# Kernel tuning notes

Hardware: AMD Instinct MI355X
Metric: run time of the kernel (lower is better)

## Reference

```python
import jax, jax.numpy as jnp
import numpy as np

B, T, F, D = 128, 128, 128, 512
SCALE = 0.05  # keep relu-LSTM activations bounded with random weights


def setup_inputs() -> dict:
    key = jax.random.key(0)
    ks = jax.random.split(key, 16)
    n = jax.random.normal
    return {
        "enc_in": n(ks[0], (B, T, F), jnp.float32),
        "dec_in": n(ks[1], (B, T, F), jnp.float32),
        "enc_W0": n(ks[2], (F, 4 * D), jnp.float32) * SCALE,
        "enc_U0": n(ks[3], (D, 4 * D), jnp.float32) * SCALE,
        "enc_b0": jnp.zeros((4 * D,), jnp.float32),
        "enc_W1": n(ks[4], (D, 4 * D), jnp.float32) * SCALE,
        "enc_U1": n(ks[5], (D, 4 * D), jnp.float32) * SCALE,
        "enc_b1": jnp.zeros((4 * D,), jnp.float32),
        "dec_W0": n(ks[6], (F, 4 * D), jnp.float32) * SCALE,
        "dec_U0": n(ks[7], (D, 4 * D), jnp.float32) * SCALE,
        "dec_b0": jnp.zeros((4 * D,), jnp.float32),
        "dec_W1": n(ks[8], (D, 4 * D), jnp.float32) * SCALE,
        "dec_U1": n(ks[9], (D, 4 * D), jnp.float32) * SCALE,
        "dec_b1": jnp.zeros((4 * D,), jnp.float32),
        "dense_W": n(ks[10], (D, F), jnp.float32) * SCALE,
        "dense_b": jnp.zeros((F,), jnp.float32),
    }


def _lstm_cell(x, h, c, W, U, b):
    # Keras gate order: i, f, g(candidate), o; activation='relu', recurrent='sigmoid'
    z = x @ W + h @ U + b
    i, f, g, o = jnp.split(z, 4, axis=-1)
    i = jax.nn.sigmoid(i)
    f = jax.nn.sigmoid(f)
    g = jax.nn.relu(g)
    o = jax.nn.sigmoid(o)
    c2 = f * c + i * g
    h2 = o * jax.nn.relu(c2)
    return h2, c2


def reference(enc_in, dec_in, enc_W0, enc_U0, enc_b0, enc_W1, enc_U1, enc_b1,
              dec_W0, dec_U0, dec_b0, dec_W1, dec_U1, dec_b1, dense_W, dense_b):
    b, t, f = enc_in.shape
    d = enc_U0.shape[0]
    enc_params = [(enc_W0, enc_U0, enc_b0), (enc_W1, enc_U1, enc_b1)]
    dec_params = [(dec_W0, dec_U0, dec_b0), (dec_W1, dec_U1, dec_b1)]

    # Encoder: state (h, c) is shared/threaded across stacked layers, as in the source.
    def enc_step(carry, x_t):
        h, c = carry
        x = x_t
        for (W, U, bb) in enc_params:
            h, c = _lstm_cell(x, h, c, W, U, bb)
            x = h
        return (h, c), None

    h0 = jnp.zeros((b, d), enc_in.dtype)
    (h, c), _ = jax.lax.scan(enc_step, (h0, h0),
                             jnp.swapaxes(enc_in, 0, 1))  # [T,B,F]

    # every layer at a timestep gets the SAME initial state (previous timestep's
    # last-layer state), per the source code.
    def dec_step(carry, _):
        h, c, inp = carry
        cur = inp
        for (W, U, bb) in dec_params:
            h2, c2 = _lstm_cell(cur, h, c, W, U, bb)
            cur = h2
        out = cur @ dense_W + dense_b
        return (h2, c2, out), out

    inp0 = dec_in[:, 0, :]
    _, outs = jax.lax.scan(dec_step, (h, c, inp0), None, length=t)  # [T,B,F]
    outs = outs[::-1]  # source reverses all_outputs before concat
    return jnp.swapaxes(outs, 0, 1)  # [B,T,F]
```

## Files before the change

kernel.cpp:

```cpp
#include <hip/hip_runtime.h>


#define Bsz 128
#define Tsz 128
#define Fsz 128
#define Dsz 512
#define ND  2048
#define NBLK 256
#define NTHR 1024

#define OFF_HT0  1024
#define OFF_HT1  (OFF_HT0 + Dsz*Bsz)
#define OFF_HMT  (OFF_HT1 + Dsz*Bsz)
#define OFF_WEND (OFF_HMT + Dsz*Bsz)
#define OFF_P_EW0   OFF_WEND
#define OFF_P_EU0   (OFF_P_EW0 + Fsz*ND)
#define OFF_P_WSUM  (OFF_P_EU0 + Dsz*ND)
#define OFF_P_WDECA (OFF_P_WSUM + Dsz*ND)
#define OFF_P_DW0   (OFF_P_WDECA + Dsz*ND)
#define OFF_P_DU0   (OFF_P_DW0 + Fsz*ND)
#define OFF_P_DW1   (OFF_P_DU0 + Dsz*ND)
#define OFF_P_DU1   (OFF_P_DW1 + Dsz*ND)
#define OFF_P_BF    (OFF_P_DU1 + Dsz*ND)
#define OFF_P_DWT   (OFF_P_BF + ND)
#define WS_PACKED_FLOATS (OFF_P_DWT + Dsz*Fsz)
#define OFF_F_WSUM  OFF_WEND
#define OFF_F_WDECA (OFF_F_WSUM + Dsz*ND)
#define OFF_F_BF    (OFF_F_WDECA + Dsz*ND)
#define OFF_F_DWT   (OFF_F_BF + ND)
#define WS_FALLBACK_FLOATS (OFF_F_DWT + Dsz*Fsz)

#define NR 12

__device__ __forceinline__ float sigf(float x) {
    return 1.0f / (1.0f + __expf(-x));
}
__device__ __forceinline__ float ld_coh(const float* p) {
    return __hip_atomic_load((float*)p, __ATOMIC_RELAXED, __HIP_MEMORY_SCOPE_AGENT);
}
__device__ __forceinline__ void st_coh(float* p, float v) {
    __hip_atomic_store(p, v, __ATOMIC_RELAXED, __HIP_MEMORY_SCOPE_AGENT);
}

__device__ __forceinline__ void arrive(unsigned* slot, unsigned ep) {
    __syncthreads();
    if (threadIdx.x == 0)
        __hip_atomic_store(slot, ep, __ATOMIC_RELEASE, __HIP_MEMORY_SCOPE_AGENT);
}
__device__ __forceinline__ void wait_grp(unsigned* gslots, unsigned ep) {
    if (threadIdx.x < 64) {
        for (;;) {
            unsigned v = (threadIdx.x < 32)
                ? __hip_atomic_load(&gslots[threadIdx.x], __ATOMIC_RELAXED,
                                    __HIP_MEMORY_SCOPE_AGENT)
                : ep;
            if (__all(v >= ep)) break;
            __builtin_amdgcn_s_sleep(1);
        }
    }
    __syncthreads();
}
__device__ __forceinline__ void gbar_all(unsigned* slots, int blkid, unsigned ep) {
    __syncthreads();
    if (threadIdx.x == 0) {
        __threadfence();
        __hip_atomic_store(&slots[blkid], ep, __ATOMIC_RELEASE,
                           __HIP_MEMORY_SCOPE_AGENT);
    }
    if (threadIdx.x < 64) {
        for (;;) {
            unsigned mn = ~0u;
            #pragma unroll
            for (int q = 0; q < 4; ++q) {
                unsigned v = __hip_atomic_load(&slots[threadIdx.x * 4 + q],
                                               __ATOMIC_RELAXED, __HIP_MEMORY_SCOPE_AGENT);
                mn = min(mn, v);
            }
            if (__all(mn >= ep)) break;
            __builtin_amdgcn_s_sleep(1);
        }
        if (threadIdx.x == 0) __threadfence();
    }
    __syncthreads();
}

__device__ void pack_gate(float* dst, const float* src, int K, int kshift, int gid) {
    const int total = K * Dsz;
    for (int u = gid; u < total; u += NBLK * NTHR) {
        const int dd = u >> kshift;
        const int k = u & (K - 1);
        const float* sp = src + (size_t)k * ND + dd;
        ((float4*)dst)[u] = make_float4(sp[0], sp[Dsz], sp[2 * Dsz], sp[3 * Dsz]);
    }
}
__device__ void pack_wsum(float* dst, const float* a, const float* bsrc, int gid) {
    for (int u = gid; u < Dsz * Dsz; u += NBLK * NTHR) {
        const int dd = u >> 9, k = u & 511;
        const float* pa = a + (size_t)k * ND + dd;
        const float* pb = bsrc + (size_t)k * ND + dd;
        ((float4*)dst)[u] = make_float4(pa[0] + pb[0], pa[Dsz] + pb[Dsz],
                                        pa[2*Dsz] + pb[2*Dsz], pa[3*Dsz] + pb[3*Dsz]);
    }
}
__device__ void pack_wdeca_p(float* dst, const float* dU0, const float* dW0,
                             const float* dw, int gid) {
    for (int u = gid; u < Dsz * Dsz; u += NBLK * NTHR) {
        const int dd = u >> 9, k = u & 511;
        const float* pu = dU0 + (size_t)k * ND + dd;
        float a0 = pu[0], a1 = pu[Dsz], a2 = pu[2*Dsz], a3 = pu[3*Dsz];
        const float* dwr = dw + k * Fsz;
        for (int j = 0; j < Fsz; ++j) {
            const float wv = dwr[j];
            const float* dr = dW0 + (size_t)j * ND + dd;
            a0 += wv * dr[0]; a1 += wv * dr[Dsz];
            a2 += wv * dr[2*Dsz]; a3 += wv * dr[3*Dsz];
        }
        ((float4*)dst)[u] = make_float4(a0, a1, a2, a3);
    }
}


__device__ __forceinline__ void stageH9(float* XL, const float* HTsrc, int sr, int rbase) {
    #pragma unroll
    for (int ii = 0; ii < 4; ++ii) {
        const int i = (int)threadIdx.x + ii * NTHR;
        const int r = i >> 3, bb = i & 7;
        XL[(rbase + r) * NR + bb] = ld_coh(HTsrc + (size_t)r * Bsz + sr + bb);
    }
}
__device__ __forceinline__ void stageX9(float* XL, const float* src, int sr, int rbase) {
    const int r = (int)threadIdx.x & 127, bb = (int)threadIdx.x >> 7;
    XL[(rbase + r) * NR + bb] = src[(size_t)(sr + bb) * (Tsz * Fsz) + r];
}

#define FMA16(A0,A1,A2,A3,x4,w4) \
    A0.x += x4.x*w4.x; A0.y += x4.x*w4.y; A0.z += x4.x*w4.z; A0.w += x4.x*w4.w; \
    A1.x += x4.y*w4.x; A1.y += x4.y*w4.y; A1.z += x4.y*w4.z; A1.w += x4.y*w4.w; \
    A2.x += x4.z*w4.x; A2.y += x4.z*w4.y; A2.z += x4.z*w4.z; A2.w += x4.z*w4.w; \
    A3.x += x4.w*w4.x; A3.y += x4.w*w4.y; A3.z += x4.w*w4.z; A3.w += x4.w*w4.w;

template<int NJ>
__device__ __forceinline__ void consTv(const float4* __restrict__ Wp,
        const float* __restrict__ Xb,
        float4& A0, float4& A1, float4& A2, float4& A3)
{
    #pragma unroll 8
    for (int j = 0; j < NJ; ++j) {
        const float4 x4 = *(const float4*)(Xb + j * (32 * NR));
        const float4 w4 = Wp[j * 32];
        FMA16(A0, A1, A2, A3, x4, w4)
    }
}

__device__ __forceinline__ float dppx1(float v) {
    return v + __int_as_float(__builtin_amdgcn_mov_dpp(
        __float_as_int(v), 0xB1, 0xf, 0xf, true));
}
__device__ __forceinline__ float dppx2(float v) {
    return v + __int_as_float(__builtin_amdgcn_mov_dpp(
        __float_as_int(v), 0x4E, 0xf, 0xf, true));
}
__device__ __forceinline__ float dpphm(float v) {
    return v + __int_as_float(__builtin_amdgcn_mov_dpp(
        __float_as_int(v), 0x141, 0xf, 0xf, true));
}
#define HXCH(lo, hi, mask, cond) { \
    float s_ = (cond) ? (lo) : (hi); \
    float r_ = __shfl_xor(s_, mask); \
    if (cond) (hi) += r_; else (lo) += r_; }

__device__ __forceinline__ float4 redZ(float4 A0, float4 A1, float4 A2, float4 A3,
                                       bool khb, bool b3b)
{
    HXCH(A0.x, A2.x, 32, khb) HXCH(A0.y, A2.y, 32, khb)
    HXCH(A0.z, A2.z, 32, khb) HXCH(A0.w, A2.w, 32, khb)
    HXCH(A1.x, A3.x, 32, khb) HXCH(A1.y, A3.y, 32, khb)
    HXCH(A1.z, A3.z, 32, khb) HXCH(A1.w, A3.w, 32, khb)
    float4 B0, B1;
    B0.x = khb ? A2.x : A0.x; B0.y = khb ? A2.y : A0.y;
    B0.z = khb ? A2.z : A0.z; B0.w = khb ? A2.w : A0.w;
    B1.x = khb ? A3.x : A1.x; B1.y = khb ? A3.y : A1.y;
    B1.z = khb ? A3.z : A1.z; B1.w = khb ? A3.w : A1.w;
    HXCH(B0.x, B1.x, 8, b3b) HXCH(B0.y, B1.y, 8, b3b)
    HXCH(B0.z, B1.z, 8, b3b) HXCH(B0.w, B1.w, 8, b3b)
    float4 Z;
    Z.x = b3b ? B1.x : B0.x; Z.y = b3b ? B1.y : B0.y;
    Z.z = b3b ? B1.z : B0.z; Z.w = b3b ? B1.w : B0.w;
    Z.x = dppx1(Z.x); Z.y = dppx1(Z.y); Z.z = dppx1(Z.z); Z.w = dppx1(Z.w);
    Z.x = dppx2(Z.x); Z.y = dppx2(Z.y); Z.z = dppx2(Z.z); Z.w = dppx2(Z.w);
    Z.x = dpphm(Z.x); Z.y = dpphm(Z.y); Z.z = dpphm(Z.z); Z.w = dpphm(Z.w);
    return Z;
}

__device__ __forceinline__ float fin4b(float4 z, const float* bias, int dcol,
                                       float cprev, float& c2o) {
    float gi = sigf(z.x + bias[dcol]);
    float gf = sigf(z.y + bias[Dsz + dcol]);
    float gg = fmaxf(z.z + bias[2 * Dsz + dcol], 0.f);
    float go = sigf(z.w + bias[3 * Dsz + dcol]);
    float c2 = gf * cprev + gi * gg;
    c2o = c2;
    return go * fmaxf(c2, 0.f);
}

__device__ __forceinline__ void out_part9(const float* XL, const float* DWL, float* ORED,
                                          int xo, int koff, int wv,
                                          bool khb, bool b3b, bool own, int sown)
{
    const int ff = wv & 3, qk = wv >> 2;
    float o0 = 0.f, o1 = 0.f, o2 = 0.f, o3 = 0.f;
    const float* Xb = XL + qk * 128 * NR + xo;
    const float* Wb = DWL + ff * 512 + qk * 128 + koff;
    #pragma unroll
    for (int j = 0; j < 4; ++j) {
        const float4 x4 = *(const float4*)(Xb + j * (32 * NR));
        const float w = Wb[j * 32];
        o0 += x4.x * w; o1 += x4.y * w; o2 += x4.z * w; o3 += x4.w * w;
    }
    HXCH(o0, o2, 32, khb) HXCH(o1, o3, 32, khb)
    float p0 = khb ? o2 : o0;
    float p1 = khb ? o3 : o1;
    HXCH(p0, p1, 8, b3b)
    float o = b3b ? p1 : p0;
    o = dppx1(o); o = dppx2(o); o = dpphm(o);
    if (own) ORED[sown * 16 + ff * 4 + qk] = o;
}

__global__ void __launch_bounds__(NTHR, 1)
lstm_ae_v10(const float* enc_in, const float* dec_in,
            const float* eW0, const float* eU0, const float* eb0,
            const float* eW1, const float* eU1, const float* eb1,
            const float* dW0, const float* dU0, const float* db0,
            const float* dW1, const float* dU1, const float* db1,
            const float* dw, const float* db_, float* out, float* ws)
{
    __shared__ float XLA[1024 * NR];
    __shared__ float XLB[1024 * NR];
    __shared__ float DWL[4 * 512];
    __shared__ float OREDA[128];
    __shared__ float OREDB[128];

    unsigned* fslots = (unsigned*)ws;
    float* HT[2] = { ws + OFF_HT0, ws + OFF_HT1 };
    float* HMT = ws + OFF_HMT;

    const int blkid = blockIdx.x;
    const int grp  = blkid & 7;
    const int mem  = blkid >> 3;
    const int sgrp = mem & 7;
    const int dslc = mem >> 3;
    const int gm   = dslc * 8 + grp;
    const int chA  = sgrp * 2, chB = chA + 1;
    unsigned* gsA = (unsigned*)ws + 256 + chA * 32;
    unsigned* gsB = (unsigned*)ws + 256 + chB * 32;
    const int srA = sgrp * 16;
    const int srB = sgrp * 16 + 8;

    const int tid  = threadIdx.x;
    const int wv   = tid >> 6;
    const int lane = tid & 63;
    const int kh   = lane >> 5;
    const int qb2  = (lane >> 4) & 1;
    const int kc   = lane & 15;
    const int koff = kh * 16 + kc;
    const int dcol = grp * 64 + dslc * 16 + wv;
    const int fcol0 = grp * 16 + dslc * 4;
    const int gid  = blkid * NTHR + tid;
    const bool khb = (kh != 0);
    const bool b3b = ((kc & 8) != 0);
    const bool own = ((kc & 7) == 0);
    const int sown = qb2 * 4 + kh * 2 + ((kc >> 3) & 1);
    const int xo   = koff * NR + qb2 * 4;

    pack_gate(ws + OFF_P_EW0, eW0, Fsz, 7, gid);
    pack_gate(ws + OFF_P_EU0, eU0, Dsz, 9, gid);
    pack_wsum(ws + OFF_P_WSUM, eW1, eU1, gid);
    pack_wdeca_p(ws + OFF_P_WDECA, dU0, dW0, dw, gid);
    pack_gate(ws + OFF_P_DW0, dW0, Fsz, 7, gid);
    pack_gate(ws + OFF_P_DU0, dU0, Dsz, 9, gid);
    pack_gate(ws + OFF_P_DW1, dW1, Dsz, 9, gid);
    pack_gate(ws + OFF_P_DU1, dU1, Dsz, 9, gid);
    if (gid < ND) {
        float acc = db0[gid];
        for (int j = 0; j < Fsz; ++j) acc += db_[j] * dW0[(size_t)j * ND + gid];
        (ws + OFF_P_BF)[gid] = acc;
    }
    if (gid < Dsz * Fsz) {
        const int f = gid >> 9, k = gid & 511;
        (ws + OFF_P_DWT)[(size_t)f * Dsz + k] = dw[(size_t)k * Fsz + f];
    }
    gbar_all(fslots, blkid, 1);

    #pragma unroll
    for (int ii = 0; ii < 2; ++ii) {
        const int i = tid + ii * NTHR;
        DWL[i] = (ws + OFF_P_DWT)[(size_t)(fcol0 + (i >> 9)) * Dsz + (i & 511)];
    }
    __syncthreads();

    const float* pBF = ws + OFF_P_BF;
    const float4* W_EW0   = (const float4*)(ws + OFF_P_EW0)   + (size_t)dcol * 128 + koff;
    const float4* W_EU0   = (const float4*)(ws + OFF_P_EU0)   + (size_t)dcol * 512 + koff;
    const float4* W_WSUM  = (const float4*)(ws + OFF_P_WSUM)  + (size_t)dcol * 512 + koff;
    const float4* W_WDECA = (const float4*)(ws + OFF_P_WDECA) + (size_t)dcol * 512 + koff;
    const float4* W_DW0   = (const float4*)(ws + OFF_P_DW0)   + (size_t)dcol * 128 + koff;
    const float4* W_DU0   = (const float4*)(ws + OFF_P_DU0)   + (size_t)dcol * 512 + koff;
    const float4* W_DW1   = (const float4*)(ws + OFF_P_DW1)   + (size_t)dcol * 512 + koff;
    const float4* W_DU1   = (const float4*)(ws + OFF_P_DU1)   + (size_t)dcol * 512 + koff;

    unsigned epA = 0, epB = 0;
    int cur = 0;
    float cA = 0.f, cmA = 0.f, cB = 0.f, cmB = 0.f;
    const float4 Z4 = make_float4(0.f, 0.f, 0.f, 0.f);

    for (int t = 0; t < Tsz; ++t) {
        stageX9(XLA, enc_in + (size_t)t * Fsz, srA, 512);
        stageX9(XLB, enc_in + (size_t)t * Fsz, srB, 512);
        __syncthreads();
        {
            float4 A0 = Z4, A1 = Z4, A2 = Z4, A3 = Z4;
            consTv<4>(W_EW0, XLA + 512 * NR + xo, A0, A1, A2, A3);
            wait_grp(gsA, epA);
            stageH9(XLA, HT[cur], srA, 0);
            __syncthreads();
            consTv<16>(W_EU0, XLA + xo, A0, A1, A2, A3);
            float4 Z = redZ(A0, A1, A2, A3, khb, b3b);
            if (own) {
                float cn; float h2 = fin4b(Z, eb0, dcol, cA, cn); cmA = cn;
                st_coh(&HMT[(size_t)dcol * Bsz + srA + sown], h2);
            }
            arrive(&gsA[gm], ++epA);
        }
        {
            float4 A0 = Z4, A1 = Z4, A2 = Z4, A3 = Z4;
            consTv<4>(W_EW0, XLB + 512 * NR + xo, A0, A1, A2, A3);
            wait_grp(gsB, epB);
            stageH9(XLB, HT[cur], srB, 0);
            __syncthreads();
            consTv<16>(W_EU0, XLB + xo, A0, A1, A2, A3);
            float4 Z = redZ(A0, A1, A2, A3, khb, b3b);
            if (own) {
                float cn; float h2 = fin4b(Z, eb0, dcol, cB, cn); cmB = cn;
                st_coh(&HMT[(size_t)dcol * Bsz + srB + sown], h2);
            }
            arrive(&gsB[gm], ++epB);
        }
        {
            wait_grp(gsA, epA);
            stageH9(XLA, HMT, srA, 0);
            __syncthreads();
            float4 A0 = Z4, A1 = Z4, A2 = Z4, A3 = Z4;
            consTv<16>(W_WSUM, XLA + xo, A0, A1, A2, A3);
            float4 Z = redZ(A0, A1, A2, A3, khb, b3b);
            if (own) {
                float cn; float h2 = fin4b(Z, eb1, dcol, cmA, cn); cA = cn;
                st_coh(&HT[cur ^ 1][(size_t)dcol * Bsz + srA + sown], h2);
            }
            arrive(&gsA[gm], ++epA);
        }
        {
            wait_grp(gsB, epB);
            stageH9(XLB, HMT, srB, 0);
            __syncthreads();
            float4 A0 = Z4, A1 = Z4, A2 = Z4, A3 = Z4;
            consTv<16>(W_WSUM, XLB + xo, A0, A1, A2, A3);
            float4 Z = redZ(A0, A1, A2, A3, khb, b3b);
            if (own) {
                float cn; float h2 = fin4b(Z, eb1, dcol, cmB, cn); cB = cn;
                st_coh(&HT[cur ^ 1][(size_t)dcol * Bsz + srB + sown], h2);
            }
            arrive(&gsB[gm], ++epB);
        }
        cur ^= 1;
    }

    {
        stageX9(XLA, dec_in, srA, 512);
        stageX9(XLB, dec_in, srB, 512);
        __syncthreads();
        {
            float4 A0 = Z4, A1 = Z4, A2 = Z4, A3 = Z4;
            consTv<4>(W_DW0, XLA + 512 * NR + xo, A0, A1, A2, A3);
            wait_grp(gsA, epA);
            stageH9(XLA, HT[cur], srA, 0);
            __syncthreads();
            consTv<16>(W_DU0, XLA + xo, A0, A1, A2, A3);
            float4 Z = redZ(A0, A1, A2, A3, khb, b3b);
            if (own) {
                float cd; float h2 = fin4b(Z, db0, dcol, cA, cd);
                st_coh(&HMT[(size_t)dcol * Bsz + srA + sown], h2);
            }
            arrive(&gsA[gm], ++epA);
        }
        {
            float4 A0 = Z4, A1 = Z4, A2 = Z4, A3 = Z4;
            consTv<4>(W_DW0, XLB + 512 * NR + xo, A0, A1, A2, A3);
            wait_grp(gsB, epB);
            stageH9(XLB, HT[cur], srB, 0);
            __syncthreads();
            consTv<16>(W_DU0, XLB + xo, A0, A1, A2, A3);
            float4 Z = redZ(A0, A1, A2, A3, khb, b3b);
            if (own) {
                float cd; float h2 = fin4b(Z, db0, dcol, cB, cd);
                st_coh(&HMT[(size_t)dcol * Bsz + srB + sown], h2);
            }
            arrive(&gsB[gm], ++epB);
        }
        {
            wait_grp(gsA, epA);
            stageH9(XLA, HMT, srA, 512);
            __syncthreads();
            float4 A0 = Z4, A1 = Z4, A2 = Z4, A3 = Z4;
            consTv<16>(W_DU1, XLA + xo, A0, A1, A2, A3);
            consTv<16>(W_DW1, XLA + 512 * NR + xo, A0, A1, A2, A3);
            float4 Z = redZ(A0, A1, A2, A3, khb, b3b);
            if (own) {
                float cn; float h2 = fin4b(Z, db1, dcol, cA, cn); cA = cn;
                st_coh(&HT[cur ^ 1][(size_t)dcol * Bsz + srA + sown], h2);
            }
            arrive(&gsA[gm], ++epA);
        }
        {
            wait_grp(gsB, epB);
            stageH9(XLB, HMT, srB, 512);
            __syncthreads();
            float4 A0 = Z4, A1 = Z4, A2 = Z4, A3 = Z4;
            consTv<16>(W_DU1, XLB + xo, A0, A1, A2, A3);
            consTv<16>(W_DW1, XLB + 512 * NR + xo, A0, A1, A2, A3);
            float4 Z = redZ(A0, A1, A2, A3, khb, b3b);
            if (own) {
                float cn; float h2 = fin4b(Z, db1, dcol, cB, cn); cB = cn;
                st_coh(&HT[cur ^ 1][(size_t)dcol * Bsz + srB + sown], h2);
            }
            arrive(&gsB[gm], ++epB);
        }
        cur ^= 1;
    }

    for (int t = 1; t < Tsz; ++t) {
        const int tt = Tsz - t;
        {
            wait_grp(gsA, epA);
            stageH9(XLA, HT[cur], srA, 0);
            __syncthreads();
            float4 A0 = Z4, A1 = Z4, A2 = Z4, A3 = Z4;
            consTv<16>(W_WDECA, XLA + xo, A0, A1, A2, A3);
            out_part9(XLA, DWL, OREDA, xo, koff, wv, khb, b3b, own, sown);
            float4 Z = redZ(A0, A1, A2, A3, khb, b3b);
            if (own) {
                float cd; float h2 = fin4b(Z, pBF, dcol, cA, cd);
                st_coh(&HMT[(size_t)dcol * Bsz + srA + sown], h2);
            }
            arrive(&gsA[gm], ++epA);
            if (tid < 32) {
                const int bb = tid >> 2, ff = tid & 3;
                const int fc = fcol0 + ff;
                const float* r = OREDA + bb * 16 + ff * 4;
                float s = r[0] + r[1] + r[2] + r[3] + db_[fc];
                out[((size_t)(srA + bb) * Tsz + tt) * Fsz + fc] = s;
            }
        }
        {
            wait_grp(gsB, epB);
            stageH9(XLB, HT[cur], srB, 0);
            __syncthreads();
            float4 A0 = Z4, A1 = Z4, A2 = Z4, A3 = Z4;
            consTv<16>(W_WDECA, XLB + xo, A0, A1, A2, A3);
            out_part9(XLB, DWL, OREDB, xo, koff, wv, khb, b3b, own, sown);
            float4 Z = redZ(A0, A1, A2, A3, khb, b3b);
            if (own) {
                float cd; float h2 = fin4b(Z, pBF, dcol, cB, cd);
                st_coh(&HMT[(size_t)dcol * Bsz + srB + sown], h2);
            }
            arrive(&gsB[gm], ++epB);
            if (tid < 32) {
                const int bb = tid >> 2, ff = tid & 3;
                const int fc = fcol0 + ff;
                const float* r = OREDB + bb * 16 + ff * 4;
                float s = r[0] + r[1] + r[2] + r[3] + db_[fc];
                out[((size_t)(srB + bb) * Tsz + tt) * Fsz + fc] = s;
            }
        }
        {
            wait_grp(gsA, epA);
            stageH9(XLA, HMT, srA, 512);
            __syncthreads();
            float4 A0 = Z4, A1 = Z4, A2 = Z4, A3 = Z4;
            consTv<16>(W_DU1, XLA + xo, A0, A1, A2, A3);
            consTv<16>(W_DW1, XLA + 512 * NR + xo, A0, A1, A2, A3);
            float4 Z = redZ(A0, A1, A2, A3, khb, b3b);
            if (own) {
                float cn; float h2 = fin4b(Z, db1, dcol, cA, cn); cA = cn;
                st_coh(&HT[cur ^ 1][(size_t)dcol * Bsz + srA + sown], h2);
            }
            arrive(&gsA[gm], ++epA);
        }
        {
            wait_grp(gsB, epB);
            stageH9(XLB, HMT, srB, 512);
            __syncthreads();
            float4 A0 = Z4, A1 = Z4, A2 = Z4, A3 = Z4;
            consTv<16>(W_DU1, XLB + xo, A0, A1, A2, A3);
            consTv<16>(W_DW1, XLB + 512 * NR + xo, A0, A1, A2, A3);
            float4 Z = redZ(A0, A1, A2, A3, khb, b3b);
            if (own) {
                float cn; float h2 = fin4b(Z, db1, dcol, cB, cn); cB = cn;
                st_coh(&HT[cur ^ 1][(size_t)dcol * Bsz + srB + sown], h2);
            }
            arrive(&gsB[gm], ++epB);
        }
        cur ^= 1;
    }

    wait_grp(gsA, epA);
    stageH9(XLA, HT[cur], srA, 0);
    __syncthreads();
    out_part9(XLA, DWL, OREDA, xo, koff, wv, khb, b3b, own, sown);
    wait_grp(gsB, epB);
    stageH9(XLB, HT[cur], srB, 0);
    __syncthreads();
    out_part9(XLB, DWL, OREDB, xo, koff, wv, khb, b3b, own, sown);
    __syncthreads();
    if (tid < 64) {
        const int half = tid >> 5;
        const int l = tid & 31;
        const int bb = l >> 2, ff = l & 3;
        const int fc = fcol0 + ff;
        const float* ored = half ? OREDB : OREDA;
        const int sr = half ? srB : srA;
        const float* r = ored + bb * 16 + ff * 4;
        float s = r[0] + r[1] + r[2] + r[3] + db_[fc];
        out[((size_t)(sr + bb) * Tsz + 0) * Fsz + fc] = s;
    }
}


__device__ __forceinline__ void stage_vec(float* XL, int xstr, int dstoff,
        const float* src, int row0, int ld, int klen, int c4shift) {
    const int q = klen >> 2;
    const int n4 = q * 16;
    for (int i = threadIdx.x; i < n4; i += NTHR) {
        const int row = i >> c4shift;
        const int c4 = i & (q - 1);
        float4 v = *(const float4*)(src + (size_t)(row0 + row) * ld + (c4 << 2));
        *(float4*)(XL + row * xstr + dstoff + (c4 << 2)) = v;
    }
}
__device__ __forceinline__ void stage_coh_T(float* XL, int xstr, int dstoff,
        const float* HTsrc, int row0) {
    for (int i = threadIdx.x; i < Dsz * 16; i += NTHR) {
        const int d = i >> 4;
        const int bb = i & 15;
        XL[bb * xstr + dstoff + d] = ld_coh(HTsrc + (size_t)d * Bsz + row0 + bb);
    }
}
__device__ __forceinline__ void acc_segS(float4& z, const float* xp,
                                         const float* W, int kbase, int ksub, int dcol) {
    for (int j = 0; j < ksub; ++j) {
        const float x = xp[j];
        const float* wr = W + (size_t)(kbase + j) * ND + dcol;
        z.x += x * wr[0];
        z.y += x * wr[Dsz];
        z.z += x * wr[2 * Dsz];
        z.w += x * wr[3 * Dsz];
    }
}
__device__ __forceinline__ void reduce4(float4& z) {
    z.x += __shfl_xor(z.x, 16); z.x += __shfl_xor(z.x, 32);
    z.y += __shfl_xor(z.y, 16); z.y += __shfl_xor(z.y, 32);
    z.z += __shfl_xor(z.z, 16); z.z += __shfl_xor(z.z, 32);
    z.w += __shfl_xor(z.w, 16); z.w += __shfl_xor(z.w, 32);
}
__device__ __forceinline__ float lstm_fin(float4 z, const float* bias, int dcol,
                                          float cprev, float& c2out) {
    float gi = sigf(z.x + bias[dcol]);
    float gf = sigf(z.y + bias[Dsz + dcol]);
    float gg = fmaxf(z.z + bias[2 * Dsz + dcol], 0.f);
    float go = sigf(z.w + bias[3 * Dsz + dcol]);
    float c2 = gf * cprev + gi * gg;
    c2out = c2;
    return go * fmaxf(c2, 0.f);
}
__device__ __forceinline__ void out_part(const float* XL, int xstr, float* ORED,
                                         int b, int kc, int w, int fcol,
                                         const float* dwT) {
    const int q = w >> 2;
    const float* xp = XL + b * xstr + q * 128 + kc * 32;
    const float* wt = dwT + (size_t)fcol * Dsz + q * 128 + kc * 32;
    float acc = 0.f;
    #pragma unroll
    for (int j = 0; j < 32; j += 4) {
        float4 x4 = *(const float4*)(xp + j);
        float4 w4 = *(const float4*)(wt + j);
        acc += x4.x * w4.x + x4.y * w4.y + x4.z * w4.z + x4.w * w4.w;
    }
    acc += __shfl_xor(acc, 16); acc += __shfl_xor(acc, 32);
    if ((threadIdx.x & 63) < 16) ORED[b * 16 + (w & 3) * 4 + q] = acc;
}

__global__ void __launch_bounds__(NTHR, 1)
lstm_ae_fb(const float* enc_in, const float* dec_in,
           const float* eW0, const float* eU0, const float* eb0,
           const float* eW1, const float* eU1, const float* eb1,
           const float* dW0, const float* dU0, const float* db0,
           const float* dW1, const float* dU1, const float* db1,
           const float* dw, const float* db_, float* out, float* ws)
{
    __shared__ float XL[16 * 1028];
    __shared__ float ORED[256];

    unsigned* fslots = (unsigned*)ws;
    float* HT[2] = { ws + OFF_HT0, ws + OFF_HT1 };
    float* HMT = ws + OFF_HMT;

    const int blkid = blockIdx.x;
    const int grp  = blkid & 7;
    const int mem  = blkid >> 3;
    const int sgrp = mem & 7;
    const int dslc = mem >> 3;
    const int gm   = dslc * 8 + grp;
    unsigned* gslots = (unsigned*)ws + 256 + sgrp * 64;

    const int tid  = threadIdx.x;
    const int w    = tid >> 6;
    const int lane = tid & 63;
    const int b    = lane & 15;
    const int kc   = lane >> 4;
    const int dcol = grp * 64 + dslc * 16 + w;
    const int bgl  = sgrp * 16 + b;
    const int row0 = sgrp * 16;
    const int fcol = grp * 16 + dslc * 4 + (w & 3);
    const int gid  = blkid * NTHR + tid;

    pack_wsum(ws + OFF_F_WSUM, eW1, eU1, gid);
    pack_wdeca_p(ws + OFF_F_WDECA, dU0, dW0, dw, gid);
    if (gid < ND) {
        float acc = db0[gid];
        for (int j = 0; j < Fsz; ++j) acc += db_[j] * dW0[(size_t)j * ND + gid];
        (ws + OFF_F_BF)[gid] = acc;
    }
    if (gid < Dsz * Fsz) {
        const int f = gid >> 9, k = gid & 511;
        (ws + OFF_F_DWT)[(size_t)f * Dsz + k] = dw[(size_t)k * Fsz + f];
    }
    const float* pWSUM = ws + OFF_F_WSUM;
    const float* pWDECA = ws + OFF_F_WDECA;
    const float* pBF = ws + OFF_F_BF;
    const float* pDWT = ws + OFF_F_DWT;
    gbar_all(fslots, blkid, 1);

    unsigned ep = 0;
    int cur = 0;
    float c_car = 0.f;

    for (int t = 0; t < Tsz; ++t) {
        stage_vec(XL, 644, 0, enc_in + (size_t)t * Fsz, row0, Tsz * Fsz, 128, 5);
        __syncthreads();
        float4 z = make_float4(0.f, 0.f, 0.f, 0.f);
        acc_segS(z, XL + b * 644 + kc * 32, eW0, kc * 32, 32, dcol);
        wait_grp(gslots, ep);
        stage_coh_T(XL, 644, 128, HT[cur], row0);
        __syncthreads();
        acc_segS(z, XL + b * 644 + 128 + kc * 128, eU0, kc * 128, 128, dcol);
        reduce4(z);
        float c1 = 0.f;
        if (lane < 16) {
            float h2 = lstm_fin(z, eb0, dcol, c_car, c1);
            st_coh(&HMT[(size_t)dcol * Bsz + bgl], h2);
        }
        arrive(&gslots[gm], ++ep);
        wait_grp(gslots, ep);
        stage_coh_T(XL, 516, 0, HMT, row0);
        __syncthreads();
        z = make_float4(0.f, 0.f, 0.f, 0.f);
        {
            const float4* wp = (const float4*)pWSUM + (size_t)dcol * 512 + kc * 128;
            const float* xp = XL + b * 516 + kc * 128;
            #pragma unroll 4
            for (int j = 0; j < 128; j += 4) {
                float4 x4 = *(const float4*)(xp + j);
                float4 w0 = wp[j], w1 = wp[j + 1], w2 = wp[j + 2], w3 = wp[j + 3];
                z.x += x4.x*w0.x + x4.y*w1.x + x4.z*w2.x + x4.w*w3.x;
                z.y += x4.x*w0.y + x4.y*w1.y + x4.z*w2.y + x4.w*w3.y;
                z.z += x4.x*w0.z + x4.y*w1.z + x4.z*w2.z + x4.w*w3.z;
                z.w += x4.x*w0.w + x4.y*w1.w + x4.z*w2.w + x4.w*w3.w;
            }
        }
        reduce4(z);
        if (lane < 16) {
            float c2;
            float h2 = lstm_fin(z, eb1, dcol, c1, c2);
            c_car = c2;
            st_coh(&HT[cur ^ 1][(size_t)dcol * Bsz + bgl], h2);
        }
        arrive(&gslots[gm], ++ep);
        cur ^= 1;
    }

    stage_vec(XL, 644, 0, dec_in, row0, Tsz * Fsz, 128, 5);
    __syncthreads();
    {
        float4 z = make_float4(0.f, 0.f, 0.f, 0.f);
        acc_segS(z, XL + b * 644 + kc * 32, dW0, kc * 32, 32, dcol);
        wait_grp(gslots, ep);
        stage_coh_T(XL, 644, 128, HT[cur], row0);
        __syncthreads();
        acc_segS(z, XL + b * 644 + 128 + kc * 128, dU0, kc * 128, 128, dcol);
        reduce4(z);
        if (lane < 16) {
            float cd;
            float h2 = lstm_fin(z, db0, dcol, c_car, cd);
            st_coh(&HMT[(size_t)dcol * Bsz + bgl], h2);
        }
        arrive(&gslots[gm], ++ep);
    }
    wait_grp(gslots, ep);
    stage_coh_T(XL, 1028, 0, HT[cur], row0);
    stage_coh_T(XL, 1028, 512, HMT, row0);
    __syncthreads();
    {
        float4 z = make_float4(0.f, 0.f, 0.f, 0.f);
        acc_segS(z, XL + b * 1028 + kc * 128, dU1, kc * 128, 128, dcol);
        acc_segS(z, XL + b * 1028 + 512 + kc * 128, dW1, kc * 128, 128, dcol);
        reduce4(z);
        if (lane < 16) {
            float c2;
            float h2 = lstm_fin(z, db1, dcol, c_car, c2);
            c_car = c2;
            st_coh(&HT[cur ^ 1][(size_t)dcol * Bsz + bgl], h2);
        }
    }
    arrive(&gslots[gm], ++ep);
    cur ^= 1;

    for (int t = 1; t < Tsz; ++t) {
        const int tt = Tsz - t;
        wait_grp(gslots, ep);
        stage_coh_T(XL, 1028, 0, HT[cur], row0);
        __syncthreads();
        {
            float4 z = make_float4(0.f, 0.f, 0.f, 0.f);
            const float4* wp = (const float4*)pWDECA + (size_t)dcol * 512 + kc * 128;
            const float* xp = XL + b * 1028 + kc * 128;
            #pragma unroll 4
            for (int j = 0; j < 128; j += 4) {
                float4 x4 = *(const float4*)(xp + j);
                float4 w0 = wp[j], w1 = wp[j + 1], w2 = wp[j + 2], w3 = wp[j + 3];
                z.x += x4.x*w0.x + x4.y*w1.x + x4.z*w2.x + x4.w*w3.x;
                z.y += x4.x*w0.y + x4.y*w1.y + x4.z*w2.y + x4.w*w3.y;
                z.z += x4.x*w0.z + x4.y*w1.z + x4.z*w2.z + x4.w*w3.z;
                z.w += x4.x*w0.w + x4.y*w1.w + x4.z*w2.w + x4.w*w3.w;
            }
            reduce4(z);
            out_part(XL, 1028, ORED, b, kc, w, fcol, pDWT);
            if (lane < 16) {
                float cd;
                float h2 = lstm_fin(z, pBF, dcol, c_car, cd);
                st_coh(&HMT[(size_t)dcol * Bsz + bgl], h2);
            }
        }
        arrive(&gslots[gm], ++ep);
        if (tid < 64) {
            const int bb = tid >> 2, ff = tid & 3;
            const int fc = grp * 16 + dslc * 4 + ff;
            const float* r = ORED + bb * 16 + ff * 4;
            float s = r[0] + r[1] + r[2] + r[3] + db_[fc];
            out[((size_t)(row0 + bb) * Tsz + tt) * Fsz + fc] = s;
        }
        wait_grp(gslots, ep);
        stage_coh_T(XL, 1028, 512, HMT, row0);
        __syncthreads();
        {
            float4 z = make_float4(0.f, 0.f, 0.f, 0.f);
            acc_segS(z, XL + b * 1028 + kc * 128, dU1, kc * 128, 128, dcol);
            acc_segS(z, XL + b * 1028 + 512 + kc * 128, dW1, kc * 128, 128, dcol);
            reduce4(z);
            if (lane < 16) {
                float c2;
                float h2 = lstm_fin(z, db1, dcol, c_car, c2);
                c_car = c2;
                st_coh(&HT[cur ^ 1][(size_t)dcol * Bsz + bgl], h2);
            }
        }
        arrive(&gslots[gm], ++ep);
        cur ^= 1;
    }

    wait_grp(gslots, ep);
    stage_coh_T(XL, 516, 0, HT[cur], row0);
    __syncthreads();
    out_part(XL, 516, ORED, b, kc, w, fcol, pDWT);
    __syncthreads();
    if (tid < 64) {
        const int bb = tid >> 2, ff = tid & 3;
        const int fc = grp * 16 + dslc * 4 + ff;
        const float* r = ORED + bb * 16 + ff * 4;
        float s = r[0] + r[1] + r[2] + r[3] + db_[fc];
        out[((size_t)(row0 + bb) * Tsz + 0) * Fsz + fc] = s;
    }
}

extern "C" void kernel_launch(void* const* d_in, const int* in_sizes, int n_in,
                              void* d_out, int out_size, void* d_ws, size_t ws_size,
                              hipStream_t stream) {
    (void)in_sizes; (void)n_in; (void)out_size;
    const float* enc_in = (const float*)d_in[0];
    const float* dec_in = (const float*)d_in[1];
    const float* eW0 = (const float*)d_in[2];
    const float* eU0 = (const float*)d_in[3];
    const float* eb0 = (const float*)d_in[4];
    const float* eW1 = (const float*)d_in[5];
    const float* eU1 = (const float*)d_in[6];
    const float* eb1 = (const float*)d_in[7];
    const float* dW0 = (const float*)d_in[8];
    const float* dU0 = (const float*)d_in[9];
    const float* db0 = (const float*)d_in[10];
    const float* dW1 = (const float*)d_in[11];
    const float* dU1 = (const float*)d_in[12];
    const float* db1 = (const float*)d_in[13];
    const float* dw  = (const float*)d_in[14];
    const float* db_ = (const float*)d_in[15];
    float* out = (float*)d_out;
    float* ws = (float*)d_ws;

    hipMemsetAsync(d_ws, 0, (size_t)(OFF_HT0 + Dsz * Bsz) * sizeof(float), stream);

    if (ws_size >= (size_t)WS_PACKED_FLOATS * sizeof(float))
        lstm_ae_v10<<<NBLK, NTHR, 0, stream>>>(
            enc_in, dec_in, eW0, eU0, eb0, eW1, eU1, eb1,
            dW0, dU0, db0, dW1, dU1, db1, dw, db_, out, ws);
    else
        lstm_ae_fb<<<NBLK, NTHR, 0, stream>>>(
            enc_in, dec_in, eW0, eU0, eb0, eW1, eU1, eb1,
            dW0, dU0, db0, dW1, dU1, db1, dw, db_, out, ws);
}
```

Before: 7.249 ms.

## Spin all waves on group barrier and prefetch recurrent weights into registers

Replaces the group wait (one wave spins, then a block-wide __syncthreads) with every wave spinning on the slot flags itself, which removes a block barrier on each recurrent step. It also prefetches the first eight float4 weight rows of the next recurrent matmul into registers before the wait, so the global weight load overlaps the barrier latency. The fallback kernel keeps the old wait inline. The cost is more register pressure and more atomic polling traffic from all waves.

```diff
diff --git a/kernel.cpp b/kernel.cpp
--- a/kernel.cpp
+++ b/kernel.cpp
@@ -47,18 +47,16 @@
     if (threadIdx.x == 0)
         __hip_atomic_store(slot, ep, __ATOMIC_RELEASE, __HIP_MEMORY_SCOPE_AGENT);
 }
-__device__ __forceinline__ void wait_grp(unsigned* gslots, unsigned ep) {
-    if (threadIdx.x < 64) {
-        for (;;) {
-            unsigned v = (threadIdx.x < 32)
-                ? __hip_atomic_load(&gslots[threadIdx.x], __ATOMIC_RELAXED,
-                                    __HIP_MEMORY_SCOPE_AGENT)
-                : ep;
-            if (__all(v >= ep)) break;
-            __builtin_amdgcn_s_sleep(1);
-        }
-    }
-    __syncthreads();
+__device__ __forceinline__ void wait_all(unsigned* gslots, unsigned ep) {
+    const int l = (int)threadIdx.x & 63;
+    for (;;) {
+        unsigned v = (l < 32)
+            ? __hip_atomic_load(&gslots[l], __ATOMIC_RELAXED,
+                                __HIP_MEMORY_SCOPE_AGENT)
+            : ep;
+        if (__all(v >= ep)) break;
+        __builtin_amdgcn_s_sleep(1);
+    }
 }
 __device__ __forceinline__ void gbar_all(unsigned* slots, int blkid, unsigned ep) {
     __syncthreads();
@@ -139,6 +137,11 @@
     A2.x += x4.z*w4.x; A2.y += x4.z*w4.y; A2.z += x4.z*w4.z; A2.w += x4.z*w4.w; \
     A3.x += x4.w*w4.x; A3.y += x4.w*w4.y; A3.z += x4.w*w4.z; A3.w += x4.w*w4.w;
 
+__device__ __forceinline__ void pref8(float4 P[8], const float4* __restrict__ Wp) {
+    #pragma unroll
+    for (int j = 0; j < 8; ++j) P[j] = Wp[j * 32];
+}
+
 template<int NJ>
 __device__ __forceinline__ void consTv(const float4* __restrict__ Wp,
         const float* __restrict__ Xb,
@@ -148,6 +151,18 @@
     for (int j = 0; j < NJ; ++j) {
         const float4 x4 = *(const float4*)(Xb + j * (32 * NR));
         const float4 w4 = Wp[j * 32];
+        FMA16(A0, A1, A2, A3, x4, w4)
+    }
+}
+template<int NJ>
+__device__ __forceinline__ void consTvP(const float4 P[8],
+        const float4* __restrict__ Wp, const float* __restrict__ Xb,
+        float4& A0, float4& A1, float4& A2, float4& A3)
+{
+    #pragma unroll
+    for (int j = 0; j < NJ; ++j) {
+        const float4 x4 = *(const float4*)(Xb + j * (32 * NR));
+        const float4 w4 = (j < 8) ? P[j] : Wp[j * 32];
         FMA16(A0, A1, A2, A3, x4, w4)
     }
 }
@@ -227,7 +242,7 @@
 }
 
 __global__ void __launch_bounds__(NTHR, 1)
-lstm_ae_v10(const float* enc_in, const float* dec_in,
+lstm_ae_v11(const float* enc_in, const float* dec_in,
             const float* eW0, const float* eU0, const float* eb0,
             const float* eW1, const float* eU1, const float* eb1,
             const float* dW0, const float* dU0, const float* db0,
@@ -312,18 +327,20 @@
     int cur = 0;
     float cA = 0.f, cmA = 0.f, cB = 0.f, cmB = 0.f;
     const float4 Z4 = make_float4(0.f, 0.f, 0.f, 0.f);
+    float4 P[8];
 
     for (int t = 0; t < Tsz; ++t) {
+        pref8(P, W_EU0);
         stageX9(XLA, enc_in + (size_t)t * Fsz, srA, 512);
         stageX9(XLB, enc_in + (size_t)t * Fsz, srB, 512);
         __syncthreads();
         {
             float4 A0 = Z4, A1 = Z4, A2 = Z4, A3 = Z4;
             consTv<4>(W_EW0, XLA + 512 * NR + xo, A0, A1, A2, A3);
-            wait_grp(gsA, epA);
+            wait_all(gsA, epA);
             stageH9(XLA, HT[cur], srA, 0);
             __syncthreads();
-            consTv<16>(W_EU0, XLA + xo, A0, A1, A2, A3);
+            consTvP<16>(P, W_EU0, XLA + xo, A0, A1, A2, A3);
             float4 Z = redZ(A0, A1, A2, A3, khb, b3b);
             if (own) {
                 float cn; float h2 = fin4b(Z, eb0, dcol, cA, cn); cmA = cn;
@@ -334,10 +351,11 @@
         {
             float4 A0 = Z4, A1 = Z4, A2 = Z4, A3 = Z4;
             consTv<4>(W_EW0, XLB + 512 * NR + xo, A0, A1, A2, A3);
-            wait_grp(gsB, epB);
+            wait_all(gsB, epB);
             stageH9(XLB, HT[cur], srB, 0);
             __syncthreads();
-            consTv<16>(W_EU0, XLB + xo, A0, A1, A2, A3);
+            consTvP<16>(P, W_EU0, XLB + xo, A0, A1, A2, A3);
+            pref8(P, W_WSUM);
             float4 Z = redZ(A0, A1, A2, A3, khb, b3b);
             if (own) {
                 float cn; float h2 = fin4b(Z, eb0, dcol, cB, cn); cmB = cn;
@@ -346,11 +364,11 @@
             arrive(&gsB[gm], ++epB);
         }
         {
-            wait_grp(gsA, epA);
+            wait_all(gsA, epA);
             stageH9(XLA, HMT, srA, 0);
             __syncthreads();
             float4 A0 = Z4, A1 = Z4, A2 = Z4, A3 = Z4;
-            consTv<16>(W_WSUM, XLA + xo, A0, A1, A2, A3);
+            consTvP<16>(P, W_WSUM, XLA + xo, A0, A1, A2, A3);
             float4 Z = redZ(A0, A1, A2, A3, khb, b3b);
             if (own) {
                 float cn; float h2 = fin4b(Z, eb1, dcol, cmA, cn); cA = cn;
@@ -359,11 +377,11 @@
             arrive(&gsA[gm], ++epA);
         }
         {
-            wait_grp(gsB, epB);
+            wait_all(gsB, epB);
             stageH9(XLB, HMT, srB, 0);
             __syncthreads();
             float4 A0 = Z4, A1 = Z4, A2 = Z4, A3 = Z4;
-            consTv<16>(W_WSUM, XLB + xo, A0, A1, A2, A3);
+            consTvP<16>(P, W_WSUM, XLB + xo, A0, A1, A2, A3);
             float4 Z = redZ(A0, A1, A2, A3, khb, b3b);
             if (own) {
                 float cn; float h2 = fin4b(Z, eb1, dcol, cmB, cn); cB = cn;
@@ -375,16 +393,17 @@
     }
 
     {
+        pref8(P, W_DU0);
         stageX9(XLA, dec_in, srA, 512);
         stageX9(XLB, dec_in, srB, 512);
         __syncthreads();
         {
             float4 A0 = Z4, A1 = Z4, A2 = Z4, A3 = Z4;
             consTv<4>(W_DW0, XLA + 512 * NR + xo, A0, A1, A2, A3);
-            wait_grp(gsA, epA);
+            wait_all(gsA, epA);
             stageH9(XLA, HT[cur], srA, 0);
             __syncthreads();
-            consTv<16>(W_DU0, XLA + xo, A0, A1, A2, A3);
+            consTvP<16>(P, W_DU0, XLA + xo, A0, A1, A2, A3);
             float4 Z = redZ(A0, A1, A2, A3, khb, b3b);
             if (own) {
                 float cd; float h2 = fin4b(Z, db0, dcol, cA, cd);
@@ -395,10 +414,11 @@
         {
             float4 A0 = Z4, A1 = Z4, A2 = Z4, A3 = Z4;
             consTv<4>(W_DW0, XLB + 512 * NR + xo, A0, A1, A2, A3);
-            wait_grp(gsB, epB);
+            wait_all(gsB, epB);
             stageH9(XLB, HT[cur], srB, 0);
             __syncthreads();
-            consTv<16>(W_DU0, XLB + xo, A0, A1, A2, A3);
+            consTvP<16>(P, W_DU0, XLB + xo, A0, A1, A2, A3);
+            pref8(P, W_DU1);
             float4 Z = redZ(A0, A1, A2, A3, khb, b3b);
             if (own) {
                 float cd; float h2 = fin4b(Z, db0, dcol, cB, cd);
@@ -407,11 +427,11 @@
             arrive(&gsB[gm], ++epB);
         }
         {
-            wait_grp(gsA, epA);
+            wait_all(gsA, epA);
             stageH9(XLA, HMT, srA, 512);
             __syncthreads();
             float4 A0 = Z4, A1 = Z4, A2 = Z4, A3 = Z4;
-            consTv<16>(W_DU1, XLA + xo, A0, A1, A2, A3);
+            consTvP<16>(P, W_DU1, XLA + xo, A0, A1, A2, A3);
             consTv<16>(W_DW1, XLA + 512 * NR + xo, A0, A1, A2, A3);
             float4 Z = redZ(A0, A1, A2, A3, khb, b3b);
             if (own) {
@@ -421,11 +441,11 @@
             arrive(&gsA[gm], ++epA);
         }
         {
-            wait_grp(gsB, epB);
+            wait_all(gsB, epB);
             stageH9(XLB, HMT, srB, 512);
             __syncthreads();
             float4 A0 = Z4, A1 = Z4, A2 = Z4, A3 = Z4;
-            consTv<16>(W_DU1, XLB + xo, A0, A1, A2, A3);
+            consTvP<16>(P, W_DU1, XLB + xo, A0, A1, A2, A3);
             consTv<16>(W_DW1, XLB + 512 * NR + xo, A0, A1, A2, A3);
             float4 Z = redZ(A0, A1, A2, A3, khb, b3b);
             if (own) {
@@ -439,12 +459,13 @@
 
     for (int t = 1; t < Tsz; ++t) {
         const int tt = Tsz - t;
-        {
-            wait_grp(gsA, epA);
+        pref8(P, W_WDECA);
+        {
+            wait_all(gsA, epA);
             stageH9(XLA, HT[cur], srA, 0);
             __syncthreads();
             float4 A0 = Z4, A1 = Z4, A2 = Z4, A3 = Z4;
-            consTv<16>(W_WDECA, XLA + xo, A0, A1, A2, A3);
+            consTvP<16>(P, W_WDECA, XLA + xo, A0, A1, A2, A3);
             out_part9(XLA, DWL, OREDA, xo, koff, wv, khb, b3b, own, sown);
             float4 Z = redZ(A0, A1, A2, A3, khb, b3b);
             if (own) {
@@ -461,11 +482,12 @@
             }
         }
         {
-            wait_grp(gsB, epB);
+            wait_all(gsB, epB);
             stageH9(XLB, HT[cur], srB, 0);
             __syncthreads();
             float4 A0 = Z4, A1 = Z4, A2 = Z4, A3 = Z4;
-            consTv<16>(W_WDECA, XLB + xo, A0, A1, A2, A3);
+            consTvP<16>(P, W_WDECA, XLB + xo, A0, A1, A2, A3);
+            pref8(P, W_DU1);
             out_part9(XLB, DWL, OREDB, xo, koff, wv, khb, b3b, own, sown);
             float4 Z = redZ(A0, A1, A2, A3, khb, b3b);
             if (own) {
@@ -482,11 +504,11 @@
             }
         }
         {
-            wait_grp(gsA, epA);
+            wait_all(gsA, epA);
             stageH9(XLA, HMT, srA, 512);
             __syncthreads();
             float4 A0 = Z4, A1 = Z4, A2 = Z4, A3 = Z4;
-            consTv<16>(W_DU1, XLA + xo, A0, A1, A2, A3);
+            consTvP<16>(P, W_DU1, XLA + xo, A0, A1, A2, A3);
             consTv<16>(W_DW1, XLA + 512 * NR + xo, A0, A1, A2, A3);
             float4 Z = redZ(A0, A1, A2, A3, khb, b3b);
             if (own) {
@@ -496,11 +518,11 @@
             arrive(&gsA[gm], ++epA);
         }
         {
-            wait_grp(gsB, epB);
+            wait_all(gsB, epB);
             stageH9(XLB, HMT, srB, 512);
             __syncthreads();
             float4 A0 = Z4, A1 = Z4, A2 = Z4, A3 = Z4;
-            consTv<16>(W_DU1, XLB + xo, A0, A1, A2, A3);
+            consTvP<16>(P, W_DU1, XLB + xo, A0, A1, A2, A3);
             consTv<16>(W_DW1, XLB + 512 * NR + xo, A0, A1, A2, A3);
             float4 Z = redZ(A0, A1, A2, A3, khb, b3b);
             if (own) {
@@ -512,11 +534,11 @@
         cur ^= 1;
     }
 
-    wait_grp(gsA, epA);
+    wait_all(gsA, epA);
     stageH9(XLA, HT[cur], srA, 0);
     __syncthreads();
     out_part9(XLA, DWL, OREDA, xo, koff, wv, khb, b3b, own, sown);
-    wait_grp(gsB, epB);
+    wait_all(gsB, epB);
     stageH9(XLB, HT[cur], srB, 0);
     __syncthreads();
     out_part9(XLB, DWL, OREDB, xo, koff, wv, khb, b3b, own, sown);
@@ -658,7 +680,17 @@
         __syncthreads();
         float4 z = make_float4(0.f, 0.f, 0.f, 0.f);
         acc_segS(z, XL + b * 644 + kc * 32, eW0, kc * 32, 32, dcol);
-        wait_grp(gslots, ep);
+        if (threadIdx.x < 64) {
+            for (;;) {
+                unsigned v = (threadIdx.x < 32)
+                    ? __hip_atomic_load(&gslots[threadIdx.x], __ATOMIC_RELAXED,
+                                        __HIP_MEMORY_SCOPE_AGENT)
+                    : ep;
+                if (__all(v >= ep)) break;
+                __builtin_amdgcn_s_sleep(1);
+            }
+        }
+        __syncthreads();
         stage_coh_T(XL, 644, 128, HT[cur], row0);
         __syncthreads();
         acc_segS(z, XL + b * 644 + 128 + kc * 128, eU0, kc * 128, 128, dcol);
@@ -669,7 +701,17 @@
             st_coh(&HMT[(size_t)dcol * Bsz + bgl], h2);
         }
         arrive(&gslots[gm], ++ep);
-        wait_grp(gslots, ep);
+        if (threadIdx.x < 64) {
+            for (;;) {
+                unsigned v = (threadIdx.x < 32)
+                    ? __hip_atomic_load(&gslots[threadIdx.x], __ATOMIC_RELAXED,
+                                        __HIP_MEMORY_SCOPE_AGENT)
+                    : ep;
+                if (__all(v >= ep)) break;
+                __builtin_amdgcn_s_sleep(1);
+            }
+        }
+        __syncthreads();
         stage_coh_T(XL, 516, 0, HMT, row0);
         __syncthreads();
         z = make_float4(0.f, 0.f, 0.f, 0.f);
@@ -702,7 +744,17 @@
     {
         float4 z = make_float4(0.f, 0.f, 0.f, 0.f);
         acc_segS(z, XL + b * 644 + kc * 32, dW0, kc * 32, 32, dcol);
-        wait_grp(gslots, ep);
+        if (threadIdx.x < 64) {
+            for (;;) {
+                unsigned v = (threadIdx.x < 32)
+                    ? __hip_atomic_load(&gslots[threadIdx.x], __ATOMIC_RELAXED,
+                                        __HIP_MEMORY_SCOPE_AGENT)
+                    : ep;
+                if (__all(v >= ep)) break;
+                __builtin_amdgcn_s_sleep(1);
+            }
+        }
+        __syncthreads();
         stage_coh_T(XL, 644, 128, HT[cur], row0);
         __syncthreads();
         acc_segS(z, XL + b * 644 + 128 + kc * 128, dU0, kc * 128, 128, dcol);
@@ -714,7 +766,17 @@
         }
         arrive(&gslots[gm], ++ep);
     }
-    wait_grp(gslots, ep);
+    if (threadIdx.x < 64) {
+        for (;;) {
+            unsigned v = (threadIdx.x < 32)
+                ? __hip_atomic_load(&gslots[threadIdx.x], __ATOMIC_RELAXED,
+                                    __HIP_MEMORY_SCOPE_AGENT)
+                : ep;
+            if (__all(v >= ep)) break;
+            __builtin_amdgcn_s_sleep(1);
+        }
+    }
+    __syncthreads();
     stage_coh_T(XL, 1028, 0, HT[cur], row0);
     stage_coh_T(XL, 1028, 512, HMT, row0);
     __syncthreads();
@@ -735,7 +797,17 @@
 
     for (int t = 1; t < Tsz; ++t) {
         const int tt = Tsz - t;
-        wait_grp(gslots, ep);
+        if (threadIdx.x < 64) {
+            for (;;) {
+                unsigned v = (threadIdx.x < 32)
+                    ? __hip_atomic_load(&gslots[threadIdx.x], __ATOMIC_RELAXED,
+                                        __HIP_MEMORY_SCOPE_AGENT)
+                    : ep;
+                if (__all(v >= ep)) break;
+                __builtin_amdgcn_s_sleep(1);
+            }
+        }
+        __syncthreads();
         stage_coh_T(XL, 1028, 0, HT[cur], row0);
         __syncthreads();
         {
@@ -767,7 +839,17 @@
             float s = r[0] + r[1] + r[2] + r[3] + db_[fc];
             out[((size_t)(row0 + bb) * Tsz + tt) * Fsz + fc] = s;
         }
-        wait_grp(gslots, ep);
+        if (threadIdx.x < 64) {
+            for (;;) {
+                unsigned v = (threadIdx.x < 32)
+                    ? __hip_atomic_load(&gslots[threadIdx.x], __ATOMIC_RELAXED,
+                                        __HIP_MEMORY_SCOPE_AGENT)
+                    : ep;
+                if (__all(v >= ep)) break;
+                __builtin_amdgcn_s_sleep(1);
+            }
+        }
+        __syncthreads();
         stage_coh_T(XL, 1028, 512, HMT, row0);
         __syncthreads();
         {
@@ -786,7 +868,17 @@
         cur ^= 1;
     }
 
-    wait_grp(gslots, ep);
+    if (threadIdx.x < 64) {
+        for (;;) {
+            unsigned v = (threadIdx.x < 32)
+                ? __hip_atomic_load(&gslots[threadIdx.x], __ATOMIC_RELAXED,
+                                    __HIP_MEMORY_SCOPE_AGENT)
+                : ep;
+            if (__all(v >= ep)) break;
+            __builtin_amdgcn_s_sleep(1);
+        }
+    }
+    __syncthreads();
     stage_coh_T(XL, 516, 0, HT[cur], row0);
     __syncthreads();
     out_part(XL, 516, ORED, b, kc, w, fcol, pDWT);
@@ -826,7 +918,7 @@
     hipMemsetAsync(d_ws, 0, (size_t)(OFF_HT0 + Dsz * Bsz) * sizeof(float), stream);
 
     if (ws_size >= (size_t)WS_PACKED_FLOATS * sizeof(float))
-        lstm_ae_v10<<<NBLK, NTHR, 0, stream>>>(
+        lstm_ae_v11<<<NBLK, NTHR, 0, stream>>>(
             enc_in, dec_in, eW0, eU0, eb0, eW1, eU1, eb1,
             dW0, dU0, db0, dW1, dU1, db1, dw, db_, out, ws);
     else
```

Measured after the change: 19.98 ms. +175.6%, slower.
